# Kernel optimization log

Measured on AMD Instinct MI355X. Metric: run time of the kernel, lower is better.

## Reference

```python
import jax, jax.numpy as jnp
import numpy as np


def setup_inputs() -> dict:
    key = jax.random.key(0)
    k1, k2, k3 = jax.random.split(key, 3)
    B, C, H, W = 16, 3, 1024, 1024
    ALPHA_MAX = 256  # 2**alpha, alpha=8
    x = jax.random.uniform(k1, (B, C, H, W), dtype=jnp.float32)
    kr = jax.random.randint(k2, (H,), 0, ALPHA_MAX, dtype=jnp.int32)
    kc = jax.random.randint(k3, (H,), 0, ALPHA_MAX, dtype=jnp.int32)
    return {"x": x, "kr": kr, "kc": kc, "iterations": 10}


def reference(x, kr, kc, iterations):
    # Rubik's-cube image encryption (Loukhaoukha et al. 2012), vectorized.
    B, C, H, W = x.shape
    xi = (x * 255.0).astype(jnp.int32)  # matches (x*255.0).long()

    # encrypt passes key = -kr / -kc; shift() does key % size (Python-style mod, nonneg)
    s_r = (-kr) % H  # per-row circular shift amounts (applied along W)
    s_c = (-kc) % W  # per-col circular shift amounts (applied along H)

    jW = jnp.arange(W, dtype=jnp.int32)
    iH = jnp.arange(H, dtype=jnp.int32)

    # Xor_scramble masks (constant across iterations):
    # dim=2 with kc: even rows ^ kc[col], odd rows ^ reversed(kc)[col]
    xor_cols = jnp.where((iH % 2 == 0)[:, None], kc[None, :], kc[::-1][None, :])  # [H,W]
    # dim=3 with kr: even cols ^ kr[row], odd cols ^ reversed(kr)[row]
    xor_rows = jnp.where((jW % 2 == 0)[None, :], kr[:, None], kr[::-1][:, None])  # [H,W]

    # gather index tables: left/right circular shift of each row, up/down of each col
    idx_left = (jW[None, :] + s_r[:, None]) % W   # [H,W] new[j] = old[(j+s)%W]
    idx_right = (jW[None, :] - s_r[:, None]) % W  # [H,W]
    idx_up = (iH[:, None] + s_c[None, :]) % H     # [H,W] new[i] = old[(i+s)%H]
    idx_down = (iH[:, None] - s_c[None, :]) % H   # [H,W]

    for _ in range(iterations):
        # row shifts: M==0 -> left shift, else right shift (per b,c,row)
        Malpha = xi.sum(axis=3) % 2  # [B,C,H]
        row_idx = jnp.where((Malpha == 0)[..., None], idx_left, idx_right)  # [B,C,H,W]
        xi = jnp.take_along_axis(xi, row_idx, axis=3)
        # column shifts: M==1 -> up shift, else down shift (per b,c,col)
        Mbeta = xi.sum(axis=2) % 2  # [B,C,W]
        col_idx = jnp.where((Mbeta == 1)[:, :, None, :], idx_up, idx_down)  # [B,C,H,W]
        xi = jnp.take_along_axis(xi, col_idx, axis=2)
        # XOR cipher (both scrambles fuse into two elementwise XORs)
        xi = (xi ^ xor_cols) ^ xor_rows

    return xi.astype(jnp.float32) / 255.0
```

## Files before the change

### kernel.cpp

```cpp
#include <hip/hip_runtime.h>

#define HH 1024
#define WW 1024
#define NPLANES 48
#define ITERS 10

#define PLANE_BYTES (1 << 20)
#define PAR_WORDS (NPLANES * 32)
#define STRIPES 32


__device__ __forceinline__ unsigned int pack4f(float4 f) {
  return  (unsigned int)(f.x * 255.0f)
       | ((unsigned int)(f.y * 255.0f) << 8)
       | ((unsigned int)(f.z * 255.0f) << 16)
       | ((unsigned int)(f.w * 255.0f) << 24);
}

__global__ __launch_bounds__(256) void init_pass(
    const float* __restrict__ xin,
    unsigned char* __restrict__ dstb,
    unsigned int* __restrict__ par0)
{
  const int t = threadIdx.x;
  const int wave = t >> 6;
  const int lane = t & 63;
  const long long grow = (long long)blockIdx.x * 4 + wave;
  const long long base = grow << 10;

  const float4* src = (const float4*)(xin + base) + lane * 4;
  float4 f0 = src[0], f1 = src[1], f2 = src[2], f3 = src[3];
  uint4 wv;
  wv.x = pack4f(f0); wv.y = pack4f(f1); wv.z = pack4f(f2); wv.w = pack4f(f3);
  ((uint4*)(dstb + base))[lane] = wv;

  unsigned int px = wv.x ^ wv.y ^ wv.z ^ wv.w;
  px ^= px >> 16; px ^= px >> 8;
  const unsigned long long bal = __ballot(px & 1u);
  if (lane == 0 && (__popcll(bal) & 1))
    atomicOr(&par0[(int)(grow >> 5)], 1u << ((int)grow & 31));
}

__global__ __launch_bounds__(256, 5) void iter_pass(
    const unsigned char* __restrict__ srcb,
    unsigned char* __restrict__ dstb,
    float* __restrict__ outF,
    const int* __restrict__ kr,
    const int* __restrict__ kc,
    const unsigned int* __restrict__ parIn,
    unsigned int* __restrict__ parOut,
    unsigned int* __restrict__ pscratch,
    const int writeF32)
{
  __shared__ unsigned int tile[HH * 8];
  const int t   = threadIdx.x;
  const int bid = blockIdx.x;
  const int swz   = (bid & 7) * (NPLANES * STRIPES / 8) + (bid >> 3);
  const int plane = swz >> 5;
  const int c0    = (swz & 31) << 5;
  const unsigned int* srcdw = (const unsigned int*)(srcb + ((long long)plane << 20));
  const int wave = t >> 6, lane = t & 63;

  {
    const int k      = t & 7;
    const int rowgrp = t >> 3;
    const unsigned int* parP = parIn + plane * 32;
    unsigned int px = 0u;
    #pragma unroll 8
    for (int j = 0; j < 32; ++j) {
      const int r = rowgrp + (j << 5);
      const unsigned int pbit = (parP[r >> 5] >> (r & 31)) & 1u;
      const int krv = kr[r];
      const int e  = pbit ? krv : ((WW - krv) & (WW - 1));
      const int o  = (c0 + e) & (WW - 1);
      const int od = o >> 2;
      const int rb = (o & 3) << 3;
      const int rbase = r << 8;
      const unsigned int w0 = srcdw[rbase + ((od + k) & 255)];
      const unsigned int ex = srcdw[rbase + ((od + 8) & 255)];
      unsigned int w1 = __shfl(w0, (lane & 56) | ((lane + 1) & 7));
      if (k == 7) w1 = ex;
      const unsigned int wout = rb ? ((w0 >> rb) | (w1 << (32 - rb))) : w0;
      tile[(r << 3) + k] = wout;
      px ^= wout;
    }
    px ^= __shfl_xor(px, 8);
    px ^= __shfl_xor(px, 16);
    px ^= __shfl_xor(px, 32);
    unsigned int* ps = pscratch + (size_t)bid * 32;
    if (lane < 8) ps[wave * 8 + lane] = px;
  }
  __syncthreads();

  const unsigned int* ps = pscratch + (size_t)bid * 32;
  const int g = t & 7;
  const unsigned int pw = ps[g] ^ ps[8 + g] ^ ps[16 + g] ^ ps[24 + g];
  const int cbase = c0 + 4 * g;
  int e0, e1, e2, e3;
  {
    const int k0 = kc[cbase + 0], k1 = kc[cbase + 1], k2 = kc[cbase + 2], k3 = kc[cbase + 3];
    e0 = ((pw >>  0) & 1) ? ((WW - k0) & (WW - 1)) : k0;
    e1 = ((pw >>  8) & 1) ? ((WW - k1) & (WW - 1)) : k1;
    e2 = ((pw >> 16) & 1) ? ((WW - k2) & (WW - 1)) : k2;
    e3 = ((pw >> 24) & 1) ? ((WW - k3) & (WW - 1)) : k3;
  }
  const unsigned int kcw_e = (unsigned)kc[cbase] | ((unsigned)kc[cbase + 1] << 8)
                           | ((unsigned)kc[cbase + 2] << 16) | ((unsigned)kc[cbase + 3] << 24);
  const unsigned int kcw_o = (unsigned)kc[1023 - cbase] | ((unsigned)kc[1022 - cbase] << 8)
                           | ((unsigned)kc[1021 - cbase] << 16) | ((unsigned)kc[1020 - cbase] << 24);

  const int rq = t >> 3;
  unsigned int* dstU = (unsigned int*)(dstb + ((long long)plane << 20));
  float4* dstF = (float4*)(outF + ((long long)plane << 20));
  const int widx0 = (c0 >> 2) + g;
  unsigned int pm = 0u;
  #pragma unroll 8
  for (int i = 0; i < 32; ++i) {
    const int r = rq + (i << 5);
    const unsigned int b0 = tile[(((r + e0) & (HH - 1)) << 3) + g];
    const unsigned int b1 = tile[(((r + e1) & (HH - 1)) << 3) + g];
    const unsigned int b2 = tile[(((r + e2) & (HH - 1)) << 3) + g];
    const unsigned int b3 = tile[(((r + e3) & (HH - 1)) << 3) + g];
    unsigned int val = (b0 & 0xffu) | (b1 & 0xff00u) | (b2 & 0xff0000u) | (b3 & 0xff000000u);
    const unsigned int krv = (unsigned)kr[r];
    const unsigned int krr = (unsigned)kr[1023 - r];
    const unsigned int krw = krv | (krr << 8) | (krv << 16) | (krr << 24);
    val ^= ((r & 1) ? kcw_o : kcw_e) ^ krw;
    if (!writeF32) {
      dstU[(r << 8) + widx0] = val;
      unsigned int v = val & 0x01010101u;
      v ^= v >> 16; v ^= v >> 8;
      pm |= (v & 1u) << i;
    } else {
      const float s = 1.0f / 255.0f;
      float4 f;
      f.x = (float)(val & 255u) * s;
      f.y = (float)((val >> 8) & 255u) * s;
      f.z = (float)((val >> 16) & 255u) * s;
      f.w = (float)(val >> 24) * s;
      dstF[(r << 8) + widx0] = f;
    }
  }

  if (!writeF32) {
    pm ^= __shfl_xor(pm, 1);
    pm ^= __shfl_xor(pm, 2);
    pm ^= __shfl_xor(pm, 4);
    unsigned int c0w = ((pm >> g)        & 1u) << rq;
    unsigned int c1w = ((pm >> (g + 8))  & 1u) << rq;
    unsigned int c2w = ((pm >> (g + 16)) & 1u) << rq;
    unsigned int c3w = ((pm >> (g + 24)) & 1u) << rq;
    c0w ^= __shfl_xor(c0w, 8); c0w ^= __shfl_xor(c0w, 16); c0w ^= __shfl_xor(c0w, 32);
    c1w ^= __shfl_xor(c1w, 8); c1w ^= __shfl_xor(c1w, 16); c1w ^= __shfl_xor(c1w, 32);
    c2w ^= __shfl_xor(c2w, 8); c2w ^= __shfl_xor(c2w, 16); c2w ^= __shfl_xor(c2w, 32);
    c3w ^= __shfl_xor(c3w, 8); c3w ^= __shfl_xor(c3w, 16); c3w ^= __shfl_xor(c3w, 32);
    if (lane < 8) {
      unsigned int* po = parOut + plane * 32;
      atomicXor(&po[lane],      c0w);
      atomicXor(&po[lane + 8],  c1w);
      atomicXor(&po[lane + 16], c2w);
      atomicXor(&po[lane + 24], c3w);
    }
  }
}

extern "C" void kernel_launch(void* const* d_in, const int* in_sizes, int n_in,
                              void* d_out, int out_size, void* d_ws, size_t ws_size,
                              hipStream_t stream) {
  const float* x  = (const float*)d_in[0];
  const int*   kr = (const int*)d_in[1];
  const int*   kc = (const int*)d_in[2];
  unsigned char* bufA = (unsigned char*)d_ws;
  unsigned char* bufB = bufA + (size_t)NPLANES * PLANE_BYTES;
  unsigned int*  par  = (unsigned int*)(bufB + (size_t)NPLANES * PLANE_BYTES);
  unsigned int*  pscr = par + (size_t)(ITERS + 1) * PAR_WORDS;
  float* out = (float*)d_out;

  hipMemsetAsync(par, 0, (size_t)(ITERS + 1) * PAR_WORDS * sizeof(unsigned int), stream);
  init_pass<<<NPLANES * HH / 4, 256, 0, stream>>>(x, bufA, par);

  for (int it = 0; it < ITERS; ++it) {
    const unsigned char* s = (it & 1) ? bufB : bufA;
    unsigned char*       d = (it & 1) ? bufA : bufB;
    iter_pass<<<NPLANES * STRIPES, 256, 0, stream>>>(
        s, d, out, kr, kc,
        par + (size_t)it * PAR_WORDS,
        par + (size_t)(it + 1) * PAR_WORDS,
        pscr, it == ITERS - 1 ? 1 : 0);
  }
}
```

Before: 713.2 us.

## Stage row-shift gathers via direct global-to-LDS loads and move parity scratch to LDS

```diff
diff --git a/kernel.cpp b/kernel.cpp
--- a/kernel.cpp
+++ b/kernel.cpp
@@ -9,6 +9,12 @@
 #define PAR_WORDS (NPLANES * 32)
 #define STRIPES 32
 
+
+__device__ __forceinline__ void gl2lds(const unsigned int* g, unsigned int* l) {
+  __builtin_amdgcn_global_load_lds(
+      (const __attribute__((address_space(1))) void*)g,
+      (__attribute__((address_space(3))) void*)l, 4, 0, 0);
+}
 
 __device__ __forceinline__ unsigned int pack4f(float4 f) {
   return  (unsigned int)(f.x * 255.0f)
@@ -41,7 +47,7 @@
     atomicOr(&par0[(int)(grow >> 5)], 1u << ((int)grow & 31));
 }
 
-__global__ __launch_bounds__(256, 5) void iter_pass(
+__global__ __launch_bounds__(256, 4) void iter_pass(
     const unsigned char* __restrict__ srcb,
     unsigned char* __restrict__ dstb,
     float* __restrict__ outF,
@@ -49,10 +55,13 @@
     const int* __restrict__ kc,
     const unsigned int* __restrict__ parIn,
     unsigned int* __restrict__ parOut,
-    unsigned int* __restrict__ pscratch,
     const int writeF32)
 {
   __shared__ unsigned int tile[HH * 8];
+  __shared__ unsigned int extD[HH];
+  __shared__ unsigned char rbArr[HH];
+  __shared__ unsigned int psL[32];
+
   const int t   = threadIdx.x;
   const int bid = blockIdx.x;
   const int swz   = (bid & 7) * (NPLANES * STRIPES / 8) + (bid >> 3);
@@ -60,41 +69,59 @@
   const int c0    = (swz & 31) << 5;
   const unsigned int* srcdw = (const unsigned int*)(srcb + ((long long)plane << 20));
   const int wave = t >> 6, lane = t & 63;
+  const unsigned int* parP = parIn + plane * 32;
 
   {
-    const int k      = t & 7;
-    const int rowgrp = t >> 3;
-    const unsigned int* parP = parIn + plane * 32;
-    unsigned int px = 0u;
+    const int k = t & 7;
+    const int rg = (t >> 3) & 7;
     #pragma unroll 8
     for (int j = 0; j < 32; ++j) {
-      const int r = rowgrp + (j << 5);
+      const int rowbase = wave * 8 + j * 32;
+      const int r = rowbase + rg;
       const unsigned int pbit = (parP[r >> 5] >> (r & 31)) & 1u;
       const int krv = kr[r];
       const int e  = pbit ? krv : ((WW - krv) & (WW - 1));
       const int o  = (c0 + e) & (WW - 1);
       const int od = o >> 2;
-      const int rb = (o & 3) << 3;
-      const int rbase = r << 8;
-      const unsigned int w0 = srcdw[rbase + ((od + k) & 255)];
-      const unsigned int ex = srcdw[rbase + ((od + 8) & 255)];
+      if (k == 0) rbArr[r] = (unsigned char)(o & 3);
+      gl2lds(srcdw + (r << 8) + ((od + k) & 255), &tile[rowbase << 3]);
+    }
+    #pragma unroll
+    for (int jj = 0; jj < 4; ++jj) {
+      const int rE = jj * 256 + wave * 64 + lane;
+      const unsigned int pbit = (parP[rE >> 5] >> (rE & 31)) & 1u;
+      const int krv = kr[rE];
+      const int e  = pbit ? krv : ((WW - krv) & (WW - 1));
+      const int od = ((c0 + e) & (WW - 1)) >> 2;
+      gl2lds(srcdw + (rE << 8) + ((od + 8) & 255), &extD[jj * 256 + wave * 64]);
+    }
+  }
+  __syncthreads();
+
+  {
+    const int k = t & 7;
+    unsigned int px = 0u;
+    #pragma unroll 8
+    for (int j = 0; j < 32; ++j) {
+      const int r = (t >> 3) + (j << 5);
+      const unsigned int w0 = tile[(r << 3) + k];
+      const unsigned int exw = extD[r];
       unsigned int w1 = __shfl(w0, (lane & 56) | ((lane + 1) & 7));
-      if (k == 7) w1 = ex;
-      const unsigned int wout = rb ? ((w0 >> rb) | (w1 << (32 - rb))) : w0;
+      if (k == 7) w1 = exw;
+      const int sh = ((int)rbArr[r]) << 3;
+      const unsigned int wout = sh ? ((w0 >> sh) | (w1 << (32 - sh))) : w0;
       tile[(r << 3) + k] = wout;
       px ^= wout;
     }
     px ^= __shfl_xor(px, 8);
     px ^= __shfl_xor(px, 16);
     px ^= __shfl_xor(px, 32);
-    unsigned int* ps = pscratch + (size_t)bid * 32;
-    if (lane < 8) ps[wave * 8 + lane] = px;
+    if (lane < 8) psL[wave * 8 + lane] = px;
   }
   __syncthreads();
 
-  const unsigned int* ps = pscratch + (size_t)bid * 32;
   const int g = t & 7;
-  const unsigned int pw = ps[g] ^ ps[8 + g] ^ ps[16 + g] ^ ps[24 + g];
+  const unsigned int pw = psL[g] ^ psL[8 + g] ^ psL[16 + g] ^ psL[24 + g];
   const int cbase = c0 + 4 * g;
   int e0, e1, e2, e3;
   {
@@ -173,7 +200,6 @@
   unsigned char* bufA = (unsigned char*)d_ws;
   unsigned char* bufB = bufA + (size_t)NPLANES * PLANE_BYTES;
   unsigned int*  par  = (unsigned int*)(bufB + (size_t)NPLANES * PLANE_BYTES);
-  unsigned int*  pscr = par + (size_t)(ITERS + 1) * PAR_WORDS;
   float* out = (float*)d_out;
 
   hipMemsetAsync(par, 0, (size_t)(ITERS + 1) * PAR_WORDS * sizeof(unsigned int), stream);
@@ -186,6 +212,6 @@
         s, d, out, kr, kc,
         par + (size_t)it * PAR_WORDS,
         par + (size_t)(it + 1) * PAR_WORDS,
-        pscr, it == ITERS - 1 ? 1 : 0);
-  }
-}
+        it == ITERS - 1 ? 1 : 0);
+  }
+}
```

New measurement: 882.3 us. +23.7%, slower.
